# Kernel tuning notes

Hardware: AMD Instinct MI355X
Metric: run time of the kernel (lower is better)

The kernel has to match this reference:

```python
import jax, jax.numpy as jnp
import numpy as np

HIDDEN = 2048
NUM_EXPERTS = 8
TOP_K = 2
CAPACITY_FACTOR = 1.5
B, S = 2, 2048


def setup_inputs() -> dict:
    key = jax.random.key(0)
    k0, k1, k2 = jax.random.split(key, 3)
    hidden_states = jax.random.normal(k0, (B, S, HIDDEN), dtype=jnp.float32)
    # xavier-normal init per nn.init.xavier_normal_
    std1 = float(np.sqrt(2.0 / (HIDDEN + HIDDEN)))
    std2 = float(np.sqrt(2.0 / (HIDDEN + NUM_EXPERTS)))
    w1 = jax.random.normal(k1, (HIDDEN, HIDDEN), dtype=jnp.float32) * std1
    b1 = jnp.zeros((HIDDEN,), dtype=jnp.float32)
    w2 = jax.random.normal(k2, (NUM_EXPERTS, HIDDEN), dtype=jnp.float32) * std2
    b2 = jnp.zeros((NUM_EXPERTS,), dtype=jnp.float32)
    return {"hidden_states": hidden_states, "w1": w1, "b1": b1, "w2": w2, "b2": b2}


def reference(hidden_states, w1, b1, w2, b2):
    Bs, Ss, H = hidden_states.shape
    E, K = NUM_EXPERTS, TOP_K
    T = Bs * Ss
    capacity = int(T * CAPACITY_FACTOR * K / E)

    # router MLP: Linear -> ReLU -> Linear (dropout=0 -> identity)
    h = jax.nn.relu(jnp.einsum('bsh,oh->bso', hidden_states, w1) + b1)
    router_logits = jnp.einsum('bsh,eh->bse', h, w2) + b2  # [B,S,E]
    router_probs = jax.nn.softmax(router_logits, axis=-1)

    top_k_probs, top_k_indices = jax.lax.top_k(router_probs, K)  # [B,S,K]
    top_k_probs = top_k_probs / (jnp.sum(top_k_probs, axis=-1, keepdims=True) + 1e-8)

    # dispatch/combine: tokens claim capacity slots in (b,s,k) order.
    fe = top_k_indices.reshape(-1)            # [T*K] expert id per assignment
    fp = top_k_probs.reshape(-1)              # [T*K] prob per assignment
    onehot = (fe[:, None] == jnp.arange(E)[None, :]).astype(jnp.int32)  # [T*K,E]
    cum = jnp.cumsum(onehot, axis=0)          # running per-expert counts
    pos = jnp.take_along_axis(cum, fe[:, None], axis=1)[:, 0] - 1        # slot index
    valid = pos < capacity
    pos_c = jnp.minimum(pos, capacity - 1)
    tok = jnp.arange(T * K) // K              # flat token index

    dispatch = jnp.zeros((T, E, capacity), dtype=router_probs.dtype)
    combine = jnp.zeros((T, E, capacity), dtype=router_probs.dtype)
    dispatch = dispatch.at[tok, fe, pos_c].add(valid.astype(router_probs.dtype))
    combine = combine.at[tok, fe, pos_c].add(jnp.where(valid, fp, 0.0))
    dispatch_tensor = dispatch.reshape(Bs, Ss, E, capacity)
    combine_tensor = combine.reshape(Bs, Ss, E, capacity)

    # load-balancing aux loss
    router_prob_per_expert = jnp.mean(router_probs, axis=(0, 1))          # [E]
    expert_mask = jax.nn.one_hot(top_k_indices, E, dtype=router_probs.dtype)  # [B,S,K,E]
    expert_usage_rate = jnp.mean(expert_mask, axis=(0, 1, 2))             # [E]
    aux_loss = jnp.sum(router_prob_per_expert * expert_usage_rate) * E

    return dispatch_tensor, combine_tensor, router_probs, aux_loss
```

## Files before the change

kernel.cpp:

```cpp
#include <hip/hip_runtime.h>

#define HID   2048
#define NE    8
#define NK    2
#define NTOK  4096
#define NASS  (NTOK * NK)
#define CAP   1536
#define DISP_ELEMS ((size_t)NTOK * NE * CAP)
#define KBLK  (HID / 32)
#define ZCHUNKS_PER_BLK 49152

typedef __bf16 bf16x8 __attribute__((ext_vector_type(8)));
typedef float  f32x4  __attribute__((ext_vector_type(4)));

typedef const __attribute__((address_space(1))) unsigned int GUint;
typedef       __attribute__((address_space(3))) unsigned int LUint;

__device__ __forceinline__ void gload16(const void* g, void* l) {
    __builtin_amdgcn_global_load_lds((GUint*)g, (LUint*)l, 16, 0, 0);
}

__global__ __launch_bounds__(256) void split_kernel(
    const float* __restrict__ src, __bf16* __restrict__ dst, int nblk)
{
    int g = blockIdx.x * 256 + threadIdx.x;
    if (g >= nblk * 4) return;
    int blk = g >> 2, sub = g & 3;
    const float* s = src + (size_t)blk * 32 + sub * 8;
    float x[8];
    float4 v0 = ((const float4*)s)[0], v1 = ((const float4*)s)[1];
    x[0]=v0.x; x[1]=v0.y; x[2]=v0.z; x[3]=v0.w;
    x[4]=v1.x; x[5]=v1.y; x[6]=v1.z; x[7]=v1.w;
    bf16x8 h8, l8;
#pragma unroll
    for (int j = 0; j < 8; ++j) {
        __bf16 h = (__bf16)x[j];
        h8[j] = h;
        l8[j] = (__bf16)(x[j] - (float)h);
    }
    __bf16* d = dst + (size_t)blk * 64;
    *(bf16x8*)(d + sub * 8)      = h8;
    *(bf16x8*)(d + 32 + sub * 8) = l8;
}

__global__ __launch_bounds__(256, 2) void gemm1_mfma_kernel(
    const __bf16* __restrict__ Xs,
    const __bf16* __restrict__ Ws,
    const float* __restrict__ b1, float* __restrict__ hout,
    float* __restrict__ zout)
{
    __shared__ __bf16 As[2][128 * 64];
    __shared__ __bf16 Bs[2][128 * 64];

    const int tid  = threadIdx.x;
    const int wid  = tid >> 6;
    const int lane = tid & 63;

    int wg  = blockIdx.x;
    int swz = (wg & 7) * 64 + (wg >> 3);
    const int bx = swz & 15;
    const int by = swz >> 4;
    const int brow = by * 128;
    const int bcol = bx * 128;

    const int srow   = lane >> 3;
    const int sslot  = lane & 7;

    const int wr = wid >> 1, wc = wid & 1;
    const int fr = lane & 15;
    const int fc = lane >> 4;

    f32x4* zdst = (f32x4*)zout + (size_t)blockIdx.x * ZCHUNKS_PER_BLK + tid;
    const f32x4 zz = (f32x4)0.f;

    f32x4 acc[4][4];
#pragma unroll
    for (int m = 0; m < 4; ++m)
#pragma unroll
        for (int n = 0; n < 4; ++n) acc[m][n] = (f32x4)0.f;

#define STAGE(buf, b)                                                          \
    {                                                                          \
        _Pragma("unroll")                                                      \
        for (int i = 0; i < 4; ++i) {                                          \
            int ra = wid * 32 + i * 8 + srow;                                  \
            int ca = sslot ^ (ra & 7);                                         \
            gload16(Xs + ((size_t)(brow + ra) * KBLK + (b)) * 64 + ca * 8,     \
                    &As[buf][(wid * 32 + i * 8) * 64]);                        \
            int rb = wid * 32 + i * 8 + srow;                                  \
            int cb = sslot ^ (rb & 7);                                         \
            gload16(Ws + ((size_t)(bcol + rb) * KBLK + (b)) * 64 + cb * 8,     \
                    &Bs[buf][(wid * 32 + i * 8) * 64]);                        \
        }                                                                      \
    }

    int cur = 0;
    STAGE(0, 0);
    __syncthreads();

    for (int b = 0; b < KBLK; ++b) {
        if (b + 1 < KBLK) STAGE(cur ^ 1, b + 1);

        {
            f32x4* z = zdst + (size_t)b * 768;
            __builtin_nontemporal_store(zz, z);
            __builtin_nontemporal_store(zz, z + 256);
            __builtin_nontemporal_store(zz, z + 512);
        }

        bf16x8 ah[4], al[4], bh[4], bl[4];
#pragma unroll
        for (int m = 0; m < 4; ++m) {
            int ra = wr * 64 + m * 16 + fr;
            ah[m] = *(const bf16x8*)&As[cur][ra * 64 + ((fc       ^ (ra & 7)) << 3)];
            al[m] = *(const bf16x8*)&As[cur][ra * 64 + (((4 + fc) ^ (ra & 7)) << 3)];
        }
#pragma unroll
        for (int n = 0; n < 4; ++n) {
            int rb = wc * 64 + n * 16 + fr;
            bh[n] = *(const bf16x8*)&Bs[cur][rb * 64 + ((fc       ^ (rb & 7)) << 3)];
            bl[n] = *(const bf16x8*)&Bs[cur][rb * 64 + (((4 + fc) ^ (rb & 7)) << 3)];
        }

#pragma unroll
        for (int m = 0; m < 4; ++m)
#pragma unroll
            for (int n = 0; n < 4; ++n) {
                f32x4 c = acc[m][n];
                c = __builtin_amdgcn_mfma_f32_16x16x32_bf16(ah[m], bh[n], c, 0, 0, 0);
                c = __builtin_amdgcn_mfma_f32_16x16x32_bf16(al[m], bh[n], c, 0, 0, 0);
                c = __builtin_amdgcn_mfma_f32_16x16x32_bf16(ah[m], bl[n], c, 0, 0, 0);
                acc[m][n] = c;
            }

        __syncthreads();
        cur ^= 1;
    }

#pragma unroll
    for (int m = 0; m < 4; ++m) {
#pragma unroll
        for (int n = 0; n < 4; ++n) {
            int row = brow + wr * 64 + m * 16 + fc * 4;
            int col = bcol + wc * 64 + n * 16 + fr;
            float bias = b1[col];
#pragma unroll
            for (int j = 0; j < 4; ++j) {
                float v = acc[m][n][j] + bias;
                hout[(size_t)(row + j) * HID + col] = fmaxf(v, 0.f);
            }
        }
    }
#undef STAGE
}

__global__ __launch_bounds__(256) void router_kernel(
    const float* __restrict__ hbuf, const float* __restrict__ w2,
    const float* __restrict__ b2, float* __restrict__ probs_out,
    int* __restrict__ topk_e, float* __restrict__ topk_p)
{
    const int t    = (blockIdx.x * 256 + threadIdx.x) >> 6;
    const int lane = threadIdx.x & 63;
    const float* hrow = hbuf + (size_t)t * HID;

    float acc[NE];
#pragma unroll
    for (int e = 0; e < NE; ++e) acc[e] = 0.f;

#pragma unroll
    for (int j = 0; j < HID / (64 * 4); ++j) {
        const int o = (j * 64 + lane) * 4;
        float4 hv = *(const float4*)(hrow + o);
#pragma unroll
        for (int e = 0; e < NE; ++e) {
            float4 wv = *(const float4*)(w2 + e * HID + o);
            acc[e] += hv.x * wv.x + hv.y * wv.y + hv.z * wv.z + hv.w * wv.w;
        }
    }
#pragma unroll
    for (int m = 32; m > 0; m >>= 1)
#pragma unroll
        for (int e = 0; e < NE; ++e) acc[e] += __shfl_xor(acc[e], m);

    if (lane == 0) {
        float lg[NE];
        float mx = -1e30f;
#pragma unroll
        for (int e = 0; e < NE; ++e) { lg[e] = acc[e] + b2[e]; mx = fmaxf(mx, lg[e]); }
        float sum = 0.f;
#pragma unroll
        for (int e = 0; e < NE; ++e) { lg[e] = expf(lg[e] - mx); sum += lg[e]; }
        float inv = 1.f / sum;
        float p[NE];
#pragma unroll
        for (int e = 0; e < NE; ++e) { p[e] = lg[e] * inv; probs_out[t * NE + e] = p[e]; }
        int e1 = 0;
#pragma unroll
        for (int e = 1; e < NE; ++e) if (p[e] > p[e1]) e1 = e;
        int e2 = -1;
#pragma unroll
        for (int e = 0; e < NE; ++e) if (e != e1 && (e2 < 0 || p[e] > p[e2])) e2 = e;
        float denom = p[e1] + p[e2] + 1e-8f;
        topk_e[t * NK + 0] = e1;
        topk_e[t * NK + 1] = e2;
        topk_p[t * NK + 0] = p[e1] / denom;
        topk_p[t * NK + 1] = p[e2] / denom;
    }
}

__global__ __launch_bounds__(256) void finalize_kernel(
    const int* __restrict__ topk_e, const float* __restrict__ topk_p,
    const float* __restrict__ probs, float* __restrict__ dispatch,
    float* __restrict__ combine, float* __restrict__ aux_out)
{
    const int tid = threadIdx.x;
    __shared__ int   sc[256][NE];
    __shared__ float tot[NE];
    __shared__ float rps[256][NE];

    int cnt[NE];
#pragma unroll
    for (int e = 0; e < NE; ++e) cnt[e] = 0;
    const int base = tid * 32;
    int eloc[32];
    for (int i = 0; i < 32; ++i) { eloc[i] = topk_e[base + i]; cnt[eloc[i]]++; }
#pragma unroll
    for (int e = 0; e < NE; ++e) sc[tid][e] = cnt[e];
    __syncthreads();
    if (tid < NE) {
        int run = 0;
        for (int i = 0; i < 256; ++i) { int v = sc[i][tid]; sc[i][tid] = run; run += v; }
        tot[tid] = (float)run;
    }
    __syncthreads();
    int run[NE];
#pragma unroll
    for (int e = 0; e < NE; ++e) run[e] = sc[tid][e];
    for (int i = 0; i < 32; ++i) {
        const int a = base + i;
        const int e = eloc[i];
        const int p = run[e]++;
        if (p < CAP) {
            const int t = a >> 1;
            const size_t off = ((size_t)t * NE + e) * CAP + p;
            dispatch[off] = 1.0f;
            combine[off]  = topk_p[a];
        }
    }

    float ps[NE];
#pragma unroll
    for (int e = 0; e < NE; ++e) ps[e] = 0.f;
    for (int t = tid; t < NTOK; t += 256)
#pragma unroll
        for (int e = 0; e < NE; ++e) ps[e] += probs[t * NE + e];
#pragma unroll
    for (int e = 0; e < NE; ++e) rps[tid][e] = ps[e];
    __syncthreads();
    for (int s = 128; s > 0; s >>= 1) {
        if (tid < s) {
#pragma unroll
            for (int e = 0; e < NE; ++e) rps[tid][e] += rps[tid + s][e];
        }
        __syncthreads();
    }
    if (tid == 0) {
        float aux = 0.f;
#pragma unroll
        for (int e = 0; e < NE; ++e)
            aux += (rps[0][e] / (float)NTOK) * (tot[e] / (float)NASS);
        aux_out[0] = aux * (float)NE;
    }
}

extern "C" void kernel_launch(void* const* d_in, const int* in_sizes, int n_in,
                              void* d_out, int out_size, void* d_ws, size_t ws_size,
                              hipStream_t stream)
{
    const float* X  = (const float*)d_in[0];
    const float* w1 = (const float*)d_in[1];
    const float* b1 = (const float*)d_in[2];
    const float* w2 = (const float*)d_in[3];
    const float* b2 = (const float*)d_in[4];

    float* out      = (float*)d_out;
    float* dispatch = out;
    float* combine  = out + DISP_ELEMS;
    float* probs    = out + 2 * DISP_ELEMS;
    float* aux      = out + 2 * DISP_ELEMS + (size_t)NTOK * NE;

    __bf16* Xs     = (__bf16*)d_ws;
    __bf16* Ws     = Xs + (size_t)NTOK * HID * 2;
    float*  hbuf   = (float*)(Ws + (size_t)HID * HID * 2);
    int*    topk_e = (int*)(hbuf + (size_t)NTOK * HID);
    float*  topk_p = (float*)(topk_e + NASS);

    split_kernel<<<(NTOK * KBLK * 4 + 255) / 256, 256, 0, stream>>>(X,  Xs, NTOK * KBLK);
    split_kernel<<<(HID  * KBLK * 4 + 255) / 256, 256, 0, stream>>>(w1, Ws, HID * KBLK);
    gemm1_mfma_kernel<<<512, 256, 0, stream>>>(Xs, Ws, b1, hbuf, out);
    router_kernel<<<NTOK / 4, 256, 0, stream>>>(hbuf, w2, b2, probs, topk_e, topk_p);
    finalize_kernel<<<1, 256, 0, stream>>>(topk_e, topk_p, probs, dispatch, combine, aux);
}
```

Baseline: 506.0 us.

## Single-buffer GEMM LDS, raise occupancy, merge split launches

Drops the LDS double buffer in the GEMM, halving shared memory to 32KB so launch bounds can ask for 3 blocks per CU. It also interleaves A-fragment loads with the MFMA loop to cut register pressure. The two fp32-to-bf16 split launches are merged into one. In exchange, global-to-LDS loads no longer overlap compute inside a block, so latency hiding now depends on other resident blocks.

```diff
diff --git a/kernel.cpp b/kernel.cpp
--- a/kernel.cpp
+++ b/kernel.cpp
@@ -8,6 +8,7 @@
 #define CAP   1536
 #define DISP_ELEMS ((size_t)NTOK * NE * CAP)
 #define KBLK  (HID / 32)
+#define NXBLK (NTOK * KBLK)
 #define ZCHUNKS_PER_BLK 49152
 
 typedef __bf16 bf16x8 __attribute__((ext_vector_type(8)));
@@ -21,12 +22,17 @@
 }
 
 __global__ __launch_bounds__(256) void split_kernel(
-    const float* __restrict__ src, __bf16* __restrict__ dst, int nblk)
+    const float* __restrict__ X, const float* __restrict__ W1,
+    __bf16* __restrict__ Xs, __bf16* __restrict__ Ws)
 {
     int g = blockIdx.x * 256 + threadIdx.x;
-    if (g >= nblk * 4) return;
     int blk = g >> 2, sub = g & 3;
-    const float* s = src + (size_t)blk * 32 + sub * 8;
+    const float* s;
+    __bf16* d;
+    if (blk < NXBLK) { s = X  + (size_t)blk * 32 + sub * 8;
+                       d = Xs + (size_t)blk * 64; }
+    else             { s = W1 + (size_t)(blk - NXBLK) * 32 + sub * 8;
+                       d = Ws + (size_t)(blk - NXBLK) * 64; }
     float x[8];
     float4 v0 = ((const float4*)s)[0], v1 = ((const float4*)s)[1];
     x[0]=v0.x; x[1]=v0.y; x[2]=v0.z; x[3]=v0.w;
@@ -38,19 +44,18 @@
         h8[j] = h;
         l8[j] = (__bf16)(x[j] - (float)h);
     }
-    __bf16* d = dst + (size_t)blk * 64;
     *(bf16x8*)(d + sub * 8)      = h8;
     *(bf16x8*)(d + 32 + sub * 8) = l8;
 }
 
-__global__ __launch_bounds__(256, 2) void gemm1_mfma_kernel(
+__global__ __launch_bounds__(256, 3) void gemm1_mfma_kernel(
     const __bf16* __restrict__ Xs,
     const __bf16* __restrict__ Ws,
     const float* __restrict__ b1, float* __restrict__ hout,
     float* __restrict__ zout)
 {
-    __shared__ __bf16 As[2][128 * 64];
-    __shared__ __bf16 Bs[2][128 * 64];
+    __shared__ __bf16 As[128 * 64];
+    __shared__ __bf16 Bs[128 * 64];
 
     const int tid  = threadIdx.x;
     const int wid  = tid >> 6;
@@ -79,27 +84,18 @@
 #pragma unroll
         for (int n = 0; n < 4; ++n) acc[m][n] = (f32x4)0.f;
 
-#define STAGE(buf, b)                                                          \
-    {                                                                          \
-        _Pragma("unroll")                                                      \
-        for (int i = 0; i < 4; ++i) {                                          \
-            int ra = wid * 32 + i * 8 + srow;                                  \
-            int ca = sslot ^ (ra & 7);                                         \
-            gload16(Xs + ((size_t)(brow + ra) * KBLK + (b)) * 64 + ca * 8,     \
-                    &As[buf][(wid * 32 + i * 8) * 64]);                        \
-            int rb = wid * 32 + i * 8 + srow;                                  \
-            int cb = sslot ^ (rb & 7);                                         \
-            gload16(Ws + ((size_t)(bcol + rb) * KBLK + (b)) * 64 + cb * 8,     \
-                    &Bs[buf][(wid * 32 + i * 8) * 64]);                        \
-        }                                                                      \
-    }
-
-    int cur = 0;
-    STAGE(0, 0);
-    __syncthreads();
-
     for (int b = 0; b < KBLK; ++b) {
-        if (b + 1 < KBLK) STAGE(cur ^ 1, b + 1);
+#pragma unroll
+        for (int i = 0; i < 4; ++i) {
+            int ra = wid * 32 + i * 8 + srow;
+            int ca = sslot ^ (ra & 7);
+            gload16(Xs + ((size_t)(brow + ra) * KBLK + b) * 64 + ca * 8,
+                    &As[(wid * 32 + i * 8) * 64]);
+            int cb = sslot ^ (ra & 7);
+            gload16(Ws + ((size_t)(bcol + ra) * KBLK + b) * 64 + cb * 8,
+                    &Bs[(wid * 32 + i * 8) * 64]);
+        }
+        __syncthreads();
 
         {
             f32x4* z = zdst + (size_t)b * 768;
@@ -108,33 +104,28 @@
             __builtin_nontemporal_store(zz, z + 512);
         }
 
-        bf16x8 ah[4], al[4], bh[4], bl[4];
+        bf16x8 bh[4], bl[4];
+#pragma unroll
+        for (int n = 0; n < 4; ++n) {
+            int rb = wc * 64 + n * 16 + fr;
+            bh[n] = *(const bf16x8*)&Bs[rb * 64 + ((fc       ^ (rb & 7)) << 3)];
+            bl[n] = *(const bf16x8*)&Bs[rb * 64 + (((4 + fc) ^ (rb & 7)) << 3)];
+        }
 #pragma unroll
         for (int m = 0; m < 4; ++m) {
             int ra = wr * 64 + m * 16 + fr;
-            ah[m] = *(const bf16x8*)&As[cur][ra * 64 + ((fc       ^ (ra & 7)) << 3)];
-            al[m] = *(const bf16x8*)&As[cur][ra * 64 + (((4 + fc) ^ (ra & 7)) << 3)];
-        }
-#pragma unroll
-        for (int n = 0; n < 4; ++n) {
-            int rb = wc * 64 + n * 16 + fr;
-            bh[n] = *(const bf16x8*)&Bs[cur][rb * 64 + ((fc       ^ (rb & 7)) << 3)];
-            bl[n] = *(const bf16x8*)&Bs[cur][rb * 64 + (((4 + fc) ^ (rb & 7)) << 3)];
-        }
-
-#pragma unroll
-        for (int m = 0; m < 4; ++m)
+            bf16x8 ah = *(const bf16x8*)&As[ra * 64 + ((fc       ^ (ra & 7)) << 3)];
+            bf16x8 al = *(const bf16x8*)&As[ra * 64 + (((4 + fc) ^ (ra & 7)) << 3)];
 #pragma unroll
             for (int n = 0; n < 4; ++n) {
                 f32x4 c = acc[m][n];
-                c = __builtin_amdgcn_mfma_f32_16x16x32_bf16(ah[m], bh[n], c, 0, 0, 0);
-                c = __builtin_amdgcn_mfma_f32_16x16x32_bf16(al[m], bh[n], c, 0, 0, 0);
-                c = __builtin_amdgcn_mfma_f32_16x16x32_bf16(ah[m], bl[n], c, 0, 0, 0);
+                c = __builtin_amdgcn_mfma_f32_16x16x32_bf16(ah, bh[n], c, 0, 0, 0);
+                c = __builtin_amdgcn_mfma_f32_16x16x32_bf16(al, bh[n], c, 0, 0, 0);
+                c = __builtin_amdgcn_mfma_f32_16x16x32_bf16(ah, bl[n], c, 0, 0, 0);
                 acc[m][n] = c;
             }
-
+        }
         __syncthreads();
-        cur ^= 1;
     }
 
 #pragma unroll
@@ -151,7 +142,6 @@
             }
         }
     }
-#undef STAGE
 }
 
 __global__ __launch_bounds__(256) void router_kernel(
@@ -295,8 +285,7 @@
     int*    topk_e = (int*)(hbuf + (size_t)NTOK * HID);
     float*  topk_p = (float*)(topk_e + NASS);
 
-    split_kernel<<<(NTOK * KBLK * 4 + 255) / 256, 256, 0, stream>>>(X,  Xs, NTOK * KBLK);
-    split_kernel<<<(HID  * KBLK * 4 + 255) / 256, 256, 0, stream>>>(w1, Ws, HID * KBLK);
+    split_kernel<<<((NTOK + HID) * KBLK * 4) / 256, 256, 0, stream>>>(X, w1, Xs, Ws);
     gemm1_mfma_kernel<<<512, 256, 0, stream>>>(Xs, Ws, b1, hbuf, out);
     router_kernel<<<NTOK / 4, 256, 0, stream>>>(hbuf, w2, b2, probs, topk_e, topk_p);
     finalize_kernel<<<1, 256, 0, stream>>>(topk_e, topk_p, probs, dispatch, combine, aux);
```

After: 509.3 us. About the same (+0.6%).
